# Optimization experiments

Hardware: AMD Instinct MI355X
Metric: run time of the kernel (lower is better)

## Reference

```python
import jax, jax.numpy as jnp
import numpy as np

B, L, DN, DE, DD, H = 2, 512, 512, 128, 128, 8
DK, DEH, DDH = DN // H, DE // H, DD // H
F = 2 * DK + DEH + 2 * DDH  # per-head concat feature size (176)
SLOPE = 0.2


def _kaiming(key, out_f, in_f):
    bound = np.sqrt(6.0 / ((1.0 + SLOPE ** 2) * in_f))
    return jax.random.uniform(key, (out_f, in_f), minval=-bound, maxval=bound, dtype=jnp.float32)


def lin(x, w, b):
    y = jnp.einsum('...i,oi->...o', x, w)
    return y if b is None else y + b


def setup_inputs() -> dict:
    key = jax.random.key(0)
    ks = jax.random.split(key, 16)
    inp = {
        'node_representation': jax.random.normal(ks[0], (B, L, DN), dtype=jnp.float32),
        'edge_representation': jax.random.normal(ks[1], (B, L, L, DE), dtype=jnp.float32),
        'diff_vec': jax.random.normal(ks[2], (B, L, DD), dtype=jnp.float32),
        'Wn_w': _kaiming(ks[3], DN, DN), 'Wn_b': jnp.zeros((DN,), jnp.float32),
        'We_w': _kaiming(ks[4], DE, DE), 'We_b': jnp.zeros((DE,), jnp.float32),
        'Wd_w': _kaiming(ks[5], DD, DD), 'Wd_b': jnp.zeros((DD,), jnp.float32),
        'Wh_w': _kaiming(ks[6], DK, DK), 'Wh_b': jnp.zeros((DK,), jnp.float32),
        'attn_w': _kaiming(ks[7], 1, F),
        'outn_w': _kaiming(ks[8], DN, DN), 'outn_b': jnp.zeros((DN,), jnp.float32),
        'Wn2_w': _kaiming(ks[9], DN, DN), 'Wn2_b': jnp.zeros((DN,), jnp.float32),
        'We2_w': _kaiming(ks[10], DE, DE), 'We2_b': jnp.zeros((DE,), jnp.float32),
        'Wd2_w': _kaiming(ks[11], DD, DD), 'Wd2_b': jnp.zeros((DD,), jnp.float32),
        'edge_w': _kaiming(ks[12], DEH, F), 'edge_b': jnp.zeros((DEH,), jnp.float32),
        'oute_w': _kaiming(ks[13], DE, DE), 'oute_b': jnp.zeros((DE,), jnp.float32),
    }
    return inp


def reference(node_representation, edge_representation, diff_vec,
              Wn_w, Wn_b, We_w, We_b, Wd_w, Wd_b, Wh_w, Wh_b, attn_w,
              outn_w, outn_b, Wn2_w, Wn2_b, We2_w, We2_b, Wd2_w, Wd2_b,
              edge_w, edge_b, oute_w, oute_b):
    lrelu = lambda x: jax.nn.leaky_relu(x, SLOPE)

    # ---- node update (GAT-style with concat score decomposed per term) ----
    npj = lin(node_representation, Wn_w, Wn_b).reshape(B, L, H, DK)
    epj = lin(edge_representation, We_w, We_b).reshape(B, L, L, H, DEH)
    dpj = lin(diff_vec, Wd_w, Wd_b).reshape(B, L, H, DDH)
    a = attn_w[0]  # concat order: [hi, hj, edge, di, dj]
    a_hi, a_hj = a[:DK], a[DK:2 * DK]
    a_e = a[2 * DK:2 * DK + DEH]
    a_di, a_dj = a[2 * DK + DEH:2 * DK + DEH + DDH], a[-DDH:]
    # scores[b,i,j,h]
    s = (jnp.einsum('blhd,d->blh', npj, a_hi)[:, :, None, :]
         + jnp.einsum('blhd,d->blh', npj, a_hj)[:, None, :, :]
         + jnp.einsum('blmhe,e->blmh', epj, a_e)
         + jnp.einsum('blhd,d->blh', dpj, a_di)[:, :, None, :]
         + jnp.einsum('blhd,d->blh', dpj, a_dj)[:, None, :, :])
    diag = jnp.eye(L, dtype=bool)[None, :, :, None]
    s = jnp.where(diag, -jnp.inf, s)
    probs = jax.nn.softmax(lrelu(s), axis=2)  # softmax over j
    node_wh = lin(npj, Wh_w, Wh_b)  # [B,L,H,DK]
    agg = jnp.einsum('blmh,bmhd->blhd', probs, node_wh)
    new_node = (npj + lrelu(agg)).reshape(B, L, DN)
    new_node = lin(new_node, outn_w, outn_b)

    # ---- edge update (concat-linear decomposed into per-term matmuls) ----
    np2 = lin(new_node, Wn2_w, Wn2_b).reshape(B, L, H, DK)
    ep2 = lin(edge_representation, We2_w, We2_b).reshape(B, L, L, H, DEH)
    dp2 = lin(diff_vec, Wd2_w, Wd2_b).reshape(B, L, H, DDH)
    # edge concat order: [edge, hi, hj, di, dj]
    W_e = edge_w[:, :DEH]
    W_hi = edge_w[:, DEH:DEH + DK]
    W_hj = edge_w[:, DEH + DK:DEH + 2 * DK]
    W_di = edge_w[:, DEH + 2 * DK:DEH + 2 * DK + DDH]
    W_dj = edge_w[:, -DDH:]
    e_out = (jnp.einsum('blmhe,fe->blmhf', ep2, W_e)
             + jnp.einsum('blhd,fd->blhf', np2, W_hi)[:, :, None]
             + jnp.einsum('blhd,fd->blhf', np2, W_hj)[:, None]
             + jnp.einsum('blhd,fd->blhf', dp2, W_di)[:, :, None]
             + jnp.einsum('blhd,fd->blhf', dp2, W_dj)[:, None]
             + edge_b)
    new_edge = lin(e_out.reshape(B, L, L, DE), oute_w, oute_b)
    return new_node, new_edge
```

## Files before the change

### kernel.cpp

```cpp
#include <hip/hip_runtime.h>
#include <hip/hip_bf16.h>

typedef unsigned short u16;
typedef unsigned short u16x8 __attribute__((ext_vector_type(8)));
typedef __bf16 bf16x8 __attribute__((ext_vector_type(8)));
typedef float f32x4 __attribute__((ext_vector_type(4)));

#define LRS 0.2f

__device__ __forceinline__ u16 f2b(float f) {
  __hip_bfloat16 h = __float2bfloat16(f);
  return __builtin_bit_cast(u16, h);
}

template<int K, int O, int KSEG, int R>
__device__ __forceinline__ void gemm_rowsR(const float* xr, const float* W, const float* bias,
                                           float* yl, float* yg, int ygstride) {
  constexpr int KPT = K / KSEG;
  constexpr int OPP = 256 / KSEG;
  const int t = threadIdx.x;
  const int ks = t % KSEG;
  const int oi = t / KSEG;
#pragma unroll
  for (int pass = 0; pass < O / OPP; ++pass) {
    const int o = pass * OPP + oi;
    float a[R];
#pragma unroll
    for (int r = 0; r < R; ++r) a[r] = 0.0f;
    const float* wp = W + (size_t)o * K + ks * KPT;
    const float* xb = xr + ks * KPT;
#pragma unroll 4
    for (int kc = 0; kc < KPT; kc += 4) {
      f32x4 w4 = *(const f32x4*)(wp + kc);
#pragma unroll
      for (int r = 0; r < R; ++r) {
        f32x4 x = *(const f32x4*)(xb + r * K + kc);
#pragma unroll
        for (int j = 0; j < 4; ++j) a[r] += x[j] * w4[j];
      }
    }
#pragma unroll
    for (int d = 1; d < KSEG; d <<= 1)
#pragma unroll
      for (int r = 0; r < R; ++r) a[r] += __shfl_xor(a[r], d, 64);
    if (ks == 0) {
      float bv = bias ? bias[o] : 0.0f;
#pragma unroll
      for (int r = 0; r < R; ++r) {
        float v = a[r] + bv;
        if (yl) yl[r * O + o] = v;
        if (yg) yg[(size_t)r * ygstride + o] = v;
      }
    }
  }
}

__global__ __launch_bounds__(256) void kW1(const float* We_w, const float* We_b, const float* attn,
                                           const float* We2_w, const float* We2_b,
                                           const float* edge_w, const float* edge_b,
                                           float* Mfull, u16* vb, float* cbe, float* sconst) {
  int gid = blockIdx.x * 256 + threadIdx.x;
  if (gid < 16384) {
    int hf = gid >> 7, c = gid & 127;
    int h = hf >> 4, fo = hf & 15;
    float s = 0;
    for (int e = 0; e < 16; ++e)
      s += edge_w[fo * 176 + e] * We2_w[(h * 16 + e) * 128 + c];
    Mfull[hf * 128 + c] = s;
  } else if (gid < 16384 + 2048) {
    int idx = gid - 16384;
    int c = idx >> 4, hc = idx & 15;
    float s = 0;
    if (hc < 8)
      for (int e = 0; e < 16; ++e)
        s += We_w[(hc * 16 + e) * 128 + c] * attn[128 + e];
    vb[c * 16 + hc] = f2b(s);
  } else if (gid < 18432 + 128) {
    int hf = gid - 18432;
    int h = hf >> 4, fo = hf & 15;
    float s = edge_b[fo];
    for (int e = 0; e < 16; ++e)
      s += We2_b[h * 16 + e] * edge_w[fo * 176 + e];
    cbe[hf] = s;
  } else if (gid < 18560 + 8) {
    int h = gid - 18560;
    float s = 0;
    for (int e = 0; e < 16; ++e)
      s += We_b[h * 16 + e] * attn[128 + e];
    sconst[h] = s;
  }
}

__global__ __launch_bounds__(256) void kW2(const float* oute_w, const float* Mfull, u16* Gb) {
  int gid = blockIdx.x * 256 + threadIdx.x;
  int o = gid >> 7, c = gid & 127;
  float s = 0;
  for (int k = 0; k < 128; ++k)
    s += oute_w[o * 128 + k] * Mfull[k * 128 + c];
  Gb[o * 128 + c] = f2b(s);
}

__global__ __launch_bounds__(256) void kN1(const float* node, const float* diff,
                                           const float* Wn_w, const float* Wn_b,
                                           const float* Wd_w, const float* Wd_b,
                                           const float* Wh_w, const float* Wh_b,
                                           const float* attn, const float* sconst,
                                           float* npj_g, float* nwh_g,
                                           float* srow_g, float* scol_g) {
  __shared__ float nrow[2 * 512], npjl[2 * 512], drow[2 * 128], dpjl[2 * 128];
  const int t = threadIdx.x;
  const int r0 = blockIdx.x * 2;
  *(f32x4*)&nrow[t * 4] = *(const f32x4*)(node + (size_t)r0 * 512 + t * 4);
  if (t < 64) *(f32x4*)&drow[t * 4] = *(const f32x4*)(diff + (size_t)r0 * 128 + t * 4);
  __syncthreads();
  gemm_rowsR<512, 512, 4, 2>(nrow, Wn_w, Wn_b, npjl, npj_g + (size_t)r0 * 512, 512);
  gemm_rowsR<128, 128, 4, 2>(drow, Wd_w, Wd_b, dpjl, nullptr, 0);
  __syncthreads();
  {
    int d = t & 63, hh = t >> 6;
#pragma unroll
    for (int hi = 0; hi < 2; ++hi) {
      int h = hh + hi * 4;
      float wb = Wh_b[d];
      float acc[2] = {wb, wb};
      for (int k = 0; k < 64; ++k) {
        float w = Wh_w[d * 64 + k];
#pragma unroll
        for (int r = 0; r < 2; ++r) acc[r] += npjl[r * 512 + h * 64 + k] * w;
      }
#pragma unroll
      for (int r = 0; r < 2; ++r) nwh_g[(size_t)(r0 + r) * 512 + h * 64 + d] = acc[r];
    }
  }
  if (t < 16) {
    int r = t >> 3, h = t & 7;
    float shi = 0, shj = 0, sdi = 0, sdj = 0;
    for (int d = 0; d < 64; ++d) {
      float x = npjl[r * 512 + h * 64 + d];
      shi += x * attn[d];
      shj += x * attn[64 + d];
    }
    for (int e = 0; e < 16; ++e) {
      float x = dpjl[r * 128 + h * 16 + e];
      sdi += x * attn[144 + e];
      sdj += x * attn[160 + e];
    }
    srow_g[(r0 + r) * 8 + h] = shi + sdi + sconst[h];
    scol_g[(r0 + r) * 8 + h] = shj + sdj;
  }
}

__global__ __launch_bounds__(256) void kA(const float* edge, const float* srow, const float* scol,
                                          const u16* vb, u16* P, float* invs, u16* abf) {
  __shared__ float smx[512 * 9];
  __shared__ float red[256];
  __shared__ float mxh8[8];
  const int bl = blockIdx.x;
  const int b = bl >> 9, l = bl & 511;
  const int t = threadIdx.x;
  const int lane = t & 63, w = t >> 6;
  const int colL = lane & 15, kg = lane >> 4;
  const int h = t & 7, seg = t >> 3;

  bf16x8 bfr[4];
#pragma unroll
  for (int ks = 0; ks < 4; ++ks) {
    u16x8 u;
#pragma unroll
    for (int j = 0; j < 8; ++j) u[j] = vb[(ks * 32 + kg * 8 + j) * 16 + colL];
    bfr[ks] = __builtin_bit_cast(bf16x8, u);
  }

  const float* eb = edge + (size_t)bl * 65536;
  u16* cb = abf ? abf + (size_t)bl * 65536 : nullptr;

  for (int ci = 0; ci < 8; ++ci) {
    const int r0 = w * 128 + ci * 16;
    const int row = r0 + colL;
    const float* rp = eb + (size_t)row * 128;
    f32x4 acc = {0, 0, 0, 0};
#pragma unroll
    for (int ks = 0; ks < 4; ++ks) {
      f32x4 e0 = *(const f32x4*)(rp + ks * 32 + kg * 8);
      f32x4 e1 = *(const f32x4*)(rp + ks * 32 + kg * 8 + 4);
      u16x8 a8;
#pragma unroll
      for (int j = 0; j < 4; ++j) { a8[j] = f2b(e0[j]); a8[4 + j] = f2b(e1[j]); }
      if (cb) *(u16x8*)(cb + (size_t)row * 128 + ks * 32 + kg * 8) = a8;
      acc = __builtin_amdgcn_mfma_f32_16x16x32_bf16(__builtin_bit_cast(bf16x8, a8), bfr[ks], acc, 0, 0, 0);
    }
    if (colL < 8) {
#pragma unroll
      for (int r = 0; r < 4; ++r)
        smx[(r0 + kg * 4 + r) * 9 + colL] = acc[r];
    }
  }
  __syncthreads();

  const float srh2 = srow[(size_t)bl * 8 + h];
  float mx = -__builtin_inff();
#pragma unroll 4
  for (int i = 0; i < 16; ++i) {
    int m = seg * 16 + i;
    float sv = smx[m * 9 + h] + srh2 + scol[((size_t)b * 512 + m) * 8 + h];
    sv = (m == l) ? -__builtin_inff() : (sv >= 0.0f ? sv : LRS * sv);
    smx[m * 9 + h] = sv;
    mx = fmaxf(mx, sv);
  }
  red[t] = mx;
  __syncthreads();
  if (t < 8) {
    float m2 = -__builtin_inff();
    for (int sg = 0; sg < 32; ++sg) m2 = fmaxf(m2, red[sg * 8 + t]);
    mxh8[t] = m2;
  }
  __syncthreads();
  float mh = mxh8[h];
  float smv = 0;
#pragma unroll 4
  for (int i = 0; i < 16; ++i) {
    int m = seg * 16 + i;
    float p = __expf(smx[m * 9 + h] - mh);
    smx[m * 9 + h] = p;
    smv += p;
  }
  red[t] = smv;
  __syncthreads();
  if (t < 8) {
    float s2 = 0;
    for (int sg = 0; sg < 32; ++sg) s2 += red[sg * 8 + t];
    invs[(size_t)bl * 8 + t] = 1.0f / s2;
  }
  __syncthreads();
#pragma unroll
  for (int k = 0; k < 2; ++k) {
    int c = k * 256 + t;
    int hp = c >> 6, mb = (c & 63) * 8;
    u16x8 pk;
#pragma unroll
    for (int j = 0; j < 8; ++j) pk[j] = f2b(smx[(mb + j) * 9 + hp]);
    *(u16x8*)(P + (((size_t)b * 8 + hp) * 512 + l) * 512 + mb) = pk;
  }
}

__global__ __launch_bounds__(256) void kAgg(const u16* P, const float* nwh, const float* npj,
                                            const float* invs, float* nnp) {
  __shared__ u16 Pt[8192];
  __shared__ u16 Vt[8192];
  const int bid = blockIdx.x;
  const int lt = bid & 7, h = (bid >> 3) & 7, b = bid >> 6;
  const int l0 = lt * 64;
  const int t = threadIdx.x;
  const int lane = t & 63, w = t >> 6;
  const int colL = lane & 15, kg = lane >> 4;

  f32x4 acc[4] = {};
  for (int mc = 0; mc < 4; ++mc) {
#pragma unroll
    for (int q = 0; q < 4; ++q) {
      int c = q * 256 + t;
      int row = c >> 4, cu = c & 15;
      u16x8 a8 = *(const u16x8*)(P + (((size_t)b * 8 + h) * 512 + l0 + row) * 512 + mc * 128 + cu * 8);
      *(u16x8*)(Pt + (row * 16 + (cu ^ (row & 7))) * 8) = a8;
    }
#pragma unroll
    for (int q = 0; q < 8; ++q) {
      int c = q * 256 + t;
      int m = c >> 4, d4 = (c & 15) * 4;
      f32x4 v = *(const f32x4*)(nwh + ((size_t)b * 512 + mc * 128 + m) * 512 + h * 64 + d4);
#pragma unroll
      for (int j = 0; j < 4; ++j) {
        int d = d4 + j;
        Vt[(d * 16 + ((m >> 3) ^ (d & 7))) * 8 + (m & 7)] = f2b(v[j]);
      }
    }
    __syncthreads();
#pragma unroll
    for (int kc = 0; kc < 4; ++kc) {
      int cu = kc * 4 + kg;
      int prow = w * 16 + colL;
      bf16x8 af = *(bf16x8*)(Pt + (prow * 16 + (cu ^ (prow & 7))) * 8);
#pragma unroll
      for (int n = 0; n < 4; ++n) {
        int d = n * 16 + colL;
        bf16x8 bf = *(bf16x8*)(Vt + (d * 16 + (cu ^ (d & 7))) * 8);
        acc[n] = __builtin_amdgcn_mfma_f32_16x16x32_bf16(af, bf, acc[n], 0, 0, 0);
      }
    }
    __syncthreads();
  }
#pragma unroll
  for (int r = 0; r < 4; ++r) {
    int l = l0 + w * 16 + kg * 4 + r;
    float iv = invs[((size_t)b * 512 + l) * 8 + h];
#pragma unroll
    for (int n = 0; n < 4; ++n) {
      int o = h * 64 + n * 16 + colL;
      size_t idx = ((size_t)b * 512 + l) * 512 + o;
      float a = acc[n][r] * iv;
      a = a >= 0.0f ? a : LRS * a;
      nnp[idx] = npj[idx] + a;
    }
  }
}

__global__ __launch_bounds__(256) void kN234(const float* nnp, const float* diff,
                                             const float* outn_w, const float* outn_b,
                                             const float* Wn2_w, const float* Wn2_b,
                                             const float* Wd2_w, const float* Wd2_b,
                                             const float* edge_w, const float* cbe,
                                             const float* oute_w, const float* oute_b,
                                             float* out0, float* Pl, float* Pm) {
  __shared__ float xr[2 * 512], o0l[2 * 512], np2l[2 * 512], dr[2 * 128], dp2l[2 * 128];
  __shared__ float Rls[2 * 128], Rms[2 * 128];
  const int t = threadIdx.x;
  const int r0 = blockIdx.x * 2;
  *(f32x4*)&xr[t * 4] = *(const f32x4*)(nnp + (size_t)r0 * 512 + t * 4);
  if (t < 64) *(f32x4*)&dr[t * 4] = *(const f32x4*)(diff + (size_t)r0 * 128 + t * 4);
  __syncthreads();
  gemm_rowsR<512, 512, 4, 2>(xr, outn_w, outn_b, o0l, out0 + (size_t)r0 * 512, 512);
  gemm_rowsR<128, 128, 4, 2>(dr, Wd2_w, Wd2_b, dp2l, nullptr, 0);
  __syncthreads();
  gemm_rowsR<512, 512, 4, 2>(o0l, Wn2_w, Wn2_b, np2l, nullptr, 0);
  __syncthreads();
  {
    int hf = t & 127, which = t >> 7;
    int h = hf >> 4, fo = hf & 15;
    const float* wh = edge_w + fo * 176 + 16 + which * 64;
    const float* wd = edge_w + fo * 176 + 144 + which * 16;
    float add = which ? 0.0f : cbe[hf];
    float* dst = which ? Rms : Rls;
#pragma unroll
    for (int r = 0; r < 2; ++r) {
      float a = add;
      for (int d = 0; d < 64; ++d) a += np2l[r * 512 + h * 64 + d] * wh[d];
      for (int e = 0; e < 16; ++e) a += dp2l[r * 128 + h * 16 + e] * wd[e];
      dst[r * 128 + hf] = a;
    }
  }
  __syncthreads();
  gemm_rowsR<128, 128, 4, 2>(Rls, oute_w, oute_b, nullptr, Pl + (size_t)r0 * 128, 128);
  gemm_rowsR<128, 128, 4, 2>(Rms, oute_w, nullptr, nullptr, Pm + (size_t)r0 * 128, 128);
}

__global__ __launch_bounds__(256) void kEc(const u16* Abf, const u16* Gb,
                                           const float* Pl, const float* Pm, float* oute) {
  __shared__ u16 At[8192];
  const int tile = blockIdx.x;
  const int bl = tile >> 3;
  const int b = bl >> 9;
  const int r0 = (tile & 7) * 64;
  const int t = threadIdx.x, lane = t & 63, w = t >> 6;
  const int colL = lane & 15, kg = lane >> 4;

  bf16x8 gf[2][4];
#pragma unroll
  for (int n = 0; n < 2; ++n)
#pragma unroll
    for (int ks = 0; ks < 4; ++ks) {
      int o = w * 32 + n * 16 + colL;
      gf[n][ks] = *(const bf16x8*)(Gb + o * 128 + ks * 32 + kg * 8);
    }
  f32x4 plv4[2];
#pragma unroll
  for (int n = 0; n < 2; ++n)
    plv4[n] = *(const f32x4*)(Pl + (size_t)bl * 128 + w * 32 + n * 16 + kg * 4);

  const u16* src = Abf + ((size_t)bl * 512 + r0) * 128;
#pragma unroll
  for (int q = 0; q < 4; ++q) {
    int c = q * 256 + t;
    int row = c >> 4, cu = c & 15;
    *(u16x8*)(At + (row * 16 + (cu ^ (row & 7))) * 8) = *(const u16x8*)(src + c * 8);
  }
  __syncthreads();

  f32x4 acc[4][2] = {};
#pragma unroll
  for (int i = 0; i < 4; ++i) {
#pragma unroll
    for (int ks = 0; ks < 4; ++ks) {
      int cu = ks * 4 + kg;
      int row = i * 16 + colL;
      bf16x8 af = *(bf16x8*)(At + (row * 16 + (cu ^ (row & 7))) * 8);
#pragma unroll
      for (int n = 0; n < 2; ++n)
        acc[i][n] = __builtin_amdgcn_mfma_f32_16x16x32_bf16(gf[n][ks], af, acc[i][n], 0, 0, 0);
    }
  }
  float* ob = oute + ((size_t)bl * 512 + r0) * 128;
#pragma unroll
  for (int i = 0; i < 4; ++i) {
    int m = i * 16 + colL;
    const float* pmp = Pm + ((size_t)b * 512 + r0 + m) * 128;
    float* orow = ob + (size_t)m * 128;
#pragma unroll
    for (int n = 0; n < 2; ++n) {
      int oc = w * 32 + n * 16 + kg * 4;
      f32x4 pm4 = *(const f32x4*)(pmp + oc);
      f32x4 o4;
#pragma unroll
      for (int r = 0; r < 4; ++r) o4[r] = acc[i][n][r] + plv4[n][r] + pm4[r];
      *(f32x4*)(orow + oc) = o4;
    }
  }
}

__global__ __launch_bounds__(256) void kEd(const float* edge, const u16* Gb,
                                           const float* Pl, const float* Pm, float* oute) {
  __shared__ u16 At[8192];
  const int tile = blockIdx.x;
  const int bl = tile >> 3;
  const int b = bl >> 9;
  const int r0 = (tile & 7) * 64;
  const int t = threadIdx.x, lane = t & 63, w = t >> 6;
  const int colL = lane & 15, kg = lane >> 4;
  bf16x8 gf[2][4];
#pragma unroll
  for (int n = 0; n < 2; ++n)
#pragma unroll
    for (int ks = 0; ks < 4; ++ks) {
      int o = w * 32 + n * 16 + colL;
      gf[n][ks] = *(const bf16x8*)(Gb + o * 128 + ks * 32 + kg * 8);
    }
  f32x4 plv4[2];
#pragma unroll
  for (int n = 0; n < 2; ++n)
    plv4[n] = *(const f32x4*)(Pl + (size_t)bl * 128 + w * 32 + n * 16 + kg * 4);

  const int arow = t >> 2, aseg = t & 3;
  {
    const float* p = edge + ((size_t)bl * 512 + r0 + arow) * 128 + aseg * 32;
    f32x4 v[8];
#pragma unroll
    for (int q = 0; q < 8; ++q) v[q] = *(const f32x4*)(p + q * 4);
#pragma unroll
    for (int jj = 0; jj < 4; ++jj) {
      u16x8 a8;
#pragma unroll
      for (int j2 = 0; j2 < 4; ++j2) {
        a8[j2]     = f2b(v[2 * jj][j2]);
        a8[4 + j2] = f2b(v[2 * jj + 1][j2]);
      }
      int cu = aseg * 4 + jj;
      *(u16x8*)(At + (arow * 16 + (cu ^ (arow & 7))) * 8) = a8;
    }
  }
  __syncthreads();
  f32x4 acc[4][2] = {};
#pragma unroll
  for (int i = 0; i < 4; ++i) {
#pragma unroll
    for (int ks = 0; ks < 4; ++ks) {
      int cu = ks * 4 + kg;
      int row = i * 16 + colL;
      bf16x8 af = *(bf16x8*)(At + (row * 16 + (cu ^ (row & 7))) * 8);
#pragma unroll
      for (int n = 0; n < 2; ++n)
        acc[i][n] = __builtin_amdgcn_mfma_f32_16x16x32_bf16(gf[n][ks], af, acc[i][n], 0, 0, 0);
    }
  }
  float* ob = oute + ((size_t)bl * 512 + r0) * 128;
#pragma unroll
  for (int i = 0; i < 4; ++i) {
    int m = i * 16 + colL;
    const float* pmp = Pm + ((size_t)b * 512 + r0 + m) * 128;
    float* orow = ob + (size_t)m * 128;
#pragma unroll
    for (int n = 0; n < 2; ++n) {
      int oc = w * 32 + n * 16 + kg * 4;
      f32x4 pm4 = *(const f32x4*)(pmp + oc);
      f32x4 o4;
#pragma unroll
      for (int r = 0; r < 4; ++r) o4[r] = acc[i][n][r] + plv4[n][r] + pm4[r];
      *(f32x4*)(orow + oc) = o4;
    }
  }
}

extern "C" void kernel_launch(void* const* d_in, const int* in_sizes, int n_in,
                              void* d_out, int out_size, void* d_ws, size_t ws_size,
                              hipStream_t stream) {
  (void)in_sizes; (void)n_in; (void)out_size;
  const float* node   = (const float*)d_in[0];
  const float* edge   = (const float*)d_in[1];
  const float* diff   = (const float*)d_in[2];
  const float* Wn_w   = (const float*)d_in[3];
  const float* Wn_b   = (const float*)d_in[4];
  const float* We_w   = (const float*)d_in[5];
  const float* We_b   = (const float*)d_in[6];
  const float* Wd_w   = (const float*)d_in[7];
  const float* Wd_b   = (const float*)d_in[8];
  const float* Wh_w   = (const float*)d_in[9];
  const float* Wh_b   = (const float*)d_in[10];
  const float* attn   = (const float*)d_in[11];
  const float* outn_w = (const float*)d_in[12];
  const float* outn_b = (const float*)d_in[13];
  const float* Wn2_w  = (const float*)d_in[14];
  const float* Wn2_b  = (const float*)d_in[15];
  const float* We2_w  = (const float*)d_in[16];
  const float* We2_b  = (const float*)d_in[17];
  const float* Wd2_w  = (const float*)d_in[18];
  const float* Wd2_b  = (const float*)d_in[19];
  const float* edge_w = (const float*)d_in[20];
  const float* edge_b = (const float*)d_in[21];
  const float* oute_w = (const float*)d_in[22];
  const float* oute_b = (const float*)d_in[23];

  float* out0 = (float*)d_out;
  float* out1 = out0 + 524288;

  float* f = (float*)d_ws;
  size_t off = 0;
  auto alloc = [&](size_t n) { float* p = f + off; off += (n + 7) & ~(size_t)7; return p; };
  float* npj    = alloc(524288);
  float* nwh    = alloc(524288);
  float* srow   = alloc(8192);
  float* scol   = alloc(8192);
  float* sconst = alloc(8);
  float* cbe    = alloc(128);
  float* Mfull  = alloc(16384);
  float* nnp    = alloc(524288);
  float* Pl     = alloc(131072);
  float* Pm     = alloc(131072);
  float* invs   = alloc(8192);
  u16* vb = (u16*)(f + off); off += 1024;
  u16* Gb = (u16*)(f + off); off += 8192;
  u16* P  = (u16*)(f + off); off += 2097152;
  const size_t abf_elems = (size_t)2 * 512 * 512 * 128;
  bool cache = ws_size >= off * 4 + abf_elems * 2 + 256;
  u16* Abf = cache ? (u16*)(f + off) : nullptr;

  hipLaunchKernelGGL(kW1, dim3(73), dim3(256), 0, stream,
                     We_w, We_b, attn, We2_w, We2_b, edge_w, edge_b, Mfull, vb, cbe, sconst);
  hipLaunchKernelGGL(kW2, dim3(64), dim3(256), 0, stream, oute_w, Mfull, Gb);
  hipLaunchKernelGGL(kN1, dim3(512), dim3(256), 0, stream,
                     node, diff, Wn_w, Wn_b, Wd_w, Wd_b, Wh_w, Wh_b, attn, sconst,
                     npj, nwh, srow, scol);
  hipLaunchKernelGGL(kA, dim3(1024), dim3(256), 0, stream,
                     edge, srow, scol, vb, P, invs, Abf);
  hipLaunchKernelGGL(kAgg, dim3(128), dim3(256), 0, stream, P, nwh, npj, invs, nnp);
  hipLaunchKernelGGL(kN234, dim3(512), dim3(256), 0, stream,
                     nnp, diff, outn_w, outn_b, Wn2_w, Wn2_b, Wd2_w, Wd2_b,
                     edge_w, cbe, oute_w, oute_b, out0, Pl, Pm);
  if (cache)
    hipLaunchKernelGGL(kEc, dim3(8192), dim3(256), 0, stream, Abf, Gb, Pl, Pm, out1);
  else
    hipLaunchKernelGGL(kEd, dim3(8192), dim3(256), 0, stream, edge, Gb, Pl, Pm, out1);
}
```

Baseline: 523.0 us.

## Split edge-score kernel into FP32 row-dot pass and separate softmax kernel

```diff
diff --git a/kernel.cpp b/kernel.cpp
--- a/kernel.cpp
+++ b/kernel.cpp
@@ -58,7 +58,7 @@
 __global__ __launch_bounds__(256) void kW1(const float* We_w, const float* We_b, const float* attn,
                                            const float* We2_w, const float* We2_b,
                                            const float* edge_w, const float* edge_b,
-                                           float* Mfull, u16* vb, float* cbe, float* sconst) {
+                                           float* Mfull, float* vf, float* cbe, float* sconst) {
   int gid = blockIdx.x * 256 + threadIdx.x;
   if (gid < 16384) {
     int hf = gid >> 7, c = gid & 127;
@@ -67,23 +67,22 @@
     for (int e = 0; e < 16; ++e)
       s += edge_w[fo * 176 + e] * We2_w[(h * 16 + e) * 128 + c];
     Mfull[hf * 128 + c] = s;
-  } else if (gid < 16384 + 2048) {
+  } else if (gid < 16384 + 1024) {
     int idx = gid - 16384;
-    int c = idx >> 4, hc = idx & 15;
+    int c = idx >> 3, h = idx & 7;
     float s = 0;
-    if (hc < 8)
-      for (int e = 0; e < 16; ++e)
-        s += We_w[(hc * 16 + e) * 128 + c] * attn[128 + e];
-    vb[c * 16 + hc] = f2b(s);
-  } else if (gid < 18432 + 128) {
-    int hf = gid - 18432;
+    for (int e = 0; e < 16; ++e)
+      s += We_w[(h * 16 + e) * 128 + c] * attn[128 + e];
+    vf[c * 8 + h] = s;
+  } else if (gid < 17408 + 128) {
+    int hf = gid - 17408;
     int h = hf >> 4, fo = hf & 15;
     float s = edge_b[fo];
     for (int e = 0; e < 16; ++e)
       s += We2_b[h * 16 + e] * edge_w[fo * 176 + e];
     cbe[hf] = s;
-  } else if (gid < 18560 + 8) {
-    int h = gid - 18560;
+  } else if (gid < 17536 + 8) {
+    int h = gid - 17536;
     float s = 0;
     for (int e = 0; e < 16; ++e)
       s += We_b[h * 16 + e] * attn[128 + e];
@@ -150,53 +149,79 @@
   }
 }
 
-__global__ __launch_bounds__(256) void kA(const float* edge, const float* srow, const float* scol,
-                                          const u16* vb, u16* P, float* invs, u16* abf) {
+__global__ __launch_bounds__(256) void kS(const float* __restrict__ edge,
+                                          const float* __restrict__ vf,
+                                          float* __restrict__ se, u16* __restrict__ abf) {
+  __shared__ float vl[1024];
+  const int t = threadIdx.x;
+  *(f32x4*)&vl[t * 4] = *(const f32x4*)(vf + t * 4);
+  __syncthreads();
+  const size_t row = (size_t)blockIdx.x * 256 + t;
+  const float* rp = edge + row * 128;
+  u16* cp = abf ? abf + row * 128 : nullptr;
+  f32x4 A[8], B[8];
+#pragma unroll
+  for (int q = 0; q < 8; ++q) A[q] = *(const f32x4*)(rp + q * 4);
+#pragma unroll
+  for (int q = 0; q < 8; ++q) B[q] = *(const f32x4*)(rp + 32 + q * 4);
+  f32x4 acc0 = {0, 0, 0, 0}, acc1 = {0, 0, 0, 0};
+
+#define PROCG(BUF, CB)                                                     \
+  {                                                                        \
+    _Pragma("unroll") for (int q = 0; q < 8; ++q) {                        \
+      f32x4 v = BUF[q];                                                    \
+      int c = CB + q * 4;                                                  \
+      _Pragma("unroll") for (int j = 0; j < 4; ++j) {                      \
+        f32x4 w0 = *(const f32x4*)&vl[(c + j) * 8];                        \
+        f32x4 w1 = *(const f32x4*)&vl[(c + j) * 8 + 4];                    \
+        acc0 += v[j] * w0;                                                 \
+        acc1 += v[j] * w1;                                                 \
+      }                                                                    \
+    }                                                                      \
+    if (cp) {                                                              \
+      _Pragma("unroll") for (int q = 0; q < 8; q += 2) {                   \
+        u16x8 pk;                                                          \
+        _Pragma("unroll") for (int j = 0; j < 4; ++j) {                    \
+          pk[j] = f2b(BUF[q][j]);                                          \
+          pk[4 + j] = f2b(BUF[q + 1][j]);                                  \
+        }                                                                  \
+        *(u16x8*)(cp + CB + q * 4) = pk;                                   \
+      }                                                                    \
+    }                                                                      \
+  }
+
+  PROCG(A, 0);
+#pragma unroll
+  for (int q = 0; q < 8; ++q) A[q] = *(const f32x4*)(rp + 64 + q * 4);
+  PROCG(B, 32);
+#pragma unroll
+  for (int q = 0; q < 8; ++q) B[q] = *(const f32x4*)(rp + 96 + q * 4);
+  PROCG(A, 64);
+  PROCG(B, 96);
+#undef PROCG
+  *(f32x4*)(se + row * 8)     = acc0;
+  *(f32x4*)(se + row * 8 + 4) = acc1;
+}
+
+__global__ __launch_bounds__(256) void kSM(const float* se, const float* srow, const float* scol,
+                                           u16* P, float* invs) {
   __shared__ float smx[512 * 9];
   __shared__ float red[256];
   __shared__ float mxh8[8];
   const int bl = blockIdx.x;
   const int b = bl >> 9, l = bl & 511;
   const int t = threadIdx.x;
-  const int lane = t & 63, w = t >> 6;
-  const int colL = lane & 15, kg = lane >> 4;
   const int h = t & 7, seg = t >> 3;
-
-  bf16x8 bfr[4];
-#pragma unroll
-  for (int ks = 0; ks < 4; ++ks) {
-    u16x8 u;
-#pragma unroll
-    for (int j = 0; j < 8; ++j) u[j] = vb[(ks * 32 + kg * 8 + j) * 16 + colL];
-    bfr[ks] = __builtin_bit_cast(bf16x8, u);
-  }
-
-  const float* eb = edge + (size_t)bl * 65536;
-  u16* cb = abf ? abf + (size_t)bl * 65536 : nullptr;
-
-  for (int ci = 0; ci < 8; ++ci) {
-    const int r0 = w * 128 + ci * 16;
-    const int row = r0 + colL;
-    const float* rp = eb + (size_t)row * 128;
-    f32x4 acc = {0, 0, 0, 0};
-#pragma unroll
-    for (int ks = 0; ks < 4; ++ks) {
-      f32x4 e0 = *(const f32x4*)(rp + ks * 32 + kg * 8);
-      f32x4 e1 = *(const f32x4*)(rp + ks * 32 + kg * 8 + 4);
-      u16x8 a8;
-#pragma unroll
-      for (int j = 0; j < 4; ++j) { a8[j] = f2b(e0[j]); a8[4 + j] = f2b(e1[j]); }
-      if (cb) *(u16x8*)(cb + (size_t)row * 128 + ks * 32 + kg * 8) = a8;
-      acc = __builtin_amdgcn_mfma_f32_16x16x32_bf16(__builtin_bit_cast(bf16x8, a8), bfr[ks], acc, 0, 0, 0);
-    }
-    if (colL < 8) {
-#pragma unroll
-      for (int r = 0; r < 4; ++r)
-        smx[(r0 + kg * 4 + r) * 9 + colL] = acc[r];
-    }
-  }
-  __syncthreads();
-
+  const float* sb = se + (size_t)bl * 4096;
+#pragma unroll
+  for (int k = 0; k < 4; ++k) {
+    int idx = k * 1024 + t * 4;
+    int m = idx >> 3, hh = idx & 7;
+    f32x4 v = *(const f32x4*)(sb + idx);
+#pragma unroll
+    for (int j = 0; j < 4; ++j) smx[m * 9 + hh + j] = v[j];
+  }
+  __syncthreads();
   const float srh2 = srow[(size_t)bl * 8 + h];
   float mx = -__builtin_inff();
 #pragma unroll 4
@@ -524,21 +549,22 @@
   float* Pl     = alloc(131072);
   float* Pm     = alloc(131072);
   float* invs   = alloc(8192);
-  u16* vb = (u16*)(f + off); off += 1024;
+  float* vf     = alloc(1024);
+  float* se     = alloc(4194304);
   u16* Gb = (u16*)(f + off); off += 8192;
   u16* P  = (u16*)(f + off); off += 2097152;
   const size_t abf_elems = (size_t)2 * 512 * 512 * 128;
   bool cache = ws_size >= off * 4 + abf_elems * 2 + 256;
   u16* Abf = cache ? (u16*)(f + off) : nullptr;
 
-  hipLaunchKernelGGL(kW1, dim3(73), dim3(256), 0, stream,
-                     We_w, We_b, attn, We2_w, We2_b, edge_w, edge_b, Mfull, vb, cbe, sconst);
+  hipLaunchKernelGGL(kW1, dim3(70), dim3(256), 0, stream,
+                     We_w, We_b, attn, We2_w, We2_b, edge_w, edge_b, Mfull, vf, cbe, sconst);
   hipLaunchKernelGGL(kW2, dim3(64), dim3(256), 0, stream, oute_w, Mfull, Gb);
   hipLaunchKernelGGL(kN1, dim3(512), dim3(256), 0, stream,
                      node, diff, Wn_w, Wn_b, Wd_w, Wd_b, Wh_w, Wh_b, attn, sconst,
                      npj, nwh, srow, scol);
-  hipLaunchKernelGGL(kA, dim3(1024), dim3(256), 0, stream,
-                     edge, srow, scol, vb, P, invs, Abf);
+  hipLaunchKernelGGL(kS, dim3(2048), dim3(256), 0, stream, edge, vf, se, Abf);
+  hipLaunchKernelGGL(kSM, dim3(1024), dim3(256), 0, stream, se, srow, scol, P, invs);
   hipLaunchKernelGGL(kAgg, dim3(128), dim3(256), 0, stream, P, nwh, npj, invs, nnp);
   hipLaunchKernelGGL(kN234, dim3(512), dim3(256), 0, stream,
                      nnp, diff, outn_w, outn_b, Wn2_w, Wn2_b, Wd2_w, Wd2_b,
```

Measured after the change: 1.155 ms. 121% more time.

## Drop bf16 edge cache and double-buffer edge loads in attention kernel

Applied to the files above, without the earlier changes.

```diff
diff --git a/kernel.cpp b/kernel.cpp
--- a/kernel.cpp
+++ b/kernel.cpp
@@ -2,6 +2,7 @@
 #include <hip/hip_bf16.h>
 
 typedef unsigned short u16;
+typedef unsigned short u16x4 __attribute__((ext_vector_type(4)));
 typedef unsigned short u16x8 __attribute__((ext_vector_type(8)));
 typedef __bf16 bf16x8 __attribute__((ext_vector_type(8)));
 typedef float f32x4 __attribute__((ext_vector_type(4)));
@@ -151,7 +152,7 @@
 }
 
 __global__ __launch_bounds__(256) void kA(const float* edge, const float* srow, const float* scol,
-                                          const u16* vb, u16* P, float* invs, u16* abf) {
+                                          const u16* vb, u16* P, float* invs) {
   __shared__ float smx[512 * 9];
   __shared__ float red[256];
   __shared__ float mxh8[8];
@@ -161,6 +162,7 @@
   const int lane = t & 63, w = t >> 6;
   const int colL = lane & 15, kg = lane >> 4;
   const int h = t & 7, seg = t >> 3;
+  const int rbase = w * 128;
 
   bf16x8 bfr[4];
 #pragma unroll
@@ -172,29 +174,45 @@
   }
 
   const float* eb = edge + (size_t)bl * 65536;
-  u16* cb = abf ? abf + (size_t)bl * 65536 : nullptr;
-
-  for (int ci = 0; ci < 8; ++ci) {
-    const int r0 = w * 128 + ci * 16;
-    const int row = r0 + colL;
-    const float* rp = eb + (size_t)row * 128;
-    f32x4 acc = {0, 0, 0, 0};
-#pragma unroll
-    for (int ks = 0; ks < 4; ++ks) {
-      f32x4 e0 = *(const f32x4*)(rp + ks * 32 + kg * 8);
-      f32x4 e1 = *(const f32x4*)(rp + ks * 32 + kg * 8 + 4);
-      u16x8 a8;
-#pragma unroll
-      for (int j = 0; j < 4; ++j) { a8[j] = f2b(e0[j]); a8[4 + j] = f2b(e1[j]); }
-      if (cb) *(u16x8*)(cb + (size_t)row * 128 + ks * 32 + kg * 8) = a8;
-      acc = __builtin_amdgcn_mfma_f32_16x16x32_bf16(__builtin_bit_cast(bf16x8, a8), bfr[ks], acc, 0, 0, 0);
-    }
-    if (colL < 8) {
-#pragma unroll
-      for (int r = 0; r < 4; ++r)
-        smx[(r0 + kg * 4 + r) * 9 + colL] = acc[r];
-    }
-  }
+
+#define LOADC(BUF, CI)                                                       \
+  {                                                                          \
+    const float* rp = eb + (size_t)(rbase + (CI) * 16 + colL) * 128 + kg * 8;\
+    _Pragma("unroll") for (int ks = 0; ks < 4; ++ks) {                       \
+      BUF[2 * ks]     = *(const f32x4*)(rp + ks * 32);                       \
+      BUF[2 * ks + 1] = *(const f32x4*)(rp + ks * 32 + 4);                   \
+    }                                                                        \
+  }
+#define PROCC(BUF, CI)                                                       \
+  {                                                                          \
+    f32x4 acc = {0, 0, 0, 0};                                                \
+    _Pragma("unroll") for (int ks = 0; ks < 4; ++ks) {                       \
+      u16x8 a8;                                                              \
+      _Pragma("unroll") for (int j = 0; j < 4; ++j) {                        \
+        a8[j]     = f2b(BUF[2 * ks][j]);                                     \
+        a8[4 + j] = f2b(BUF[2 * ks + 1][j]);                                 \
+      }                                                                      \
+      acc = __builtin_amdgcn_mfma_f32_16x16x32_bf16(                         \
+          __builtin_bit_cast(bf16x8, a8), bfr[ks], acc, 0, 0, 0);            \
+    }                                                                        \
+    if (colL < 8) {                                                          \
+      _Pragma("unroll") for (int r = 0; r < 4; ++r)                          \
+        smx[(rbase + (CI) * 16 + kg * 4 + r) * 9 + colL] = acc[r];           \
+    }                                                                        \
+  }
+
+  f32x4 A[8], B[8];
+  LOADC(A, 0); LOADC(B, 1);
+  PROCC(A, 0); LOADC(A, 2);
+  PROCC(B, 1); LOADC(B, 3);
+  PROCC(A, 2); LOADC(A, 4);
+  PROCC(B, 3); LOADC(B, 5);
+  PROCC(A, 4); LOADC(A, 6);
+  PROCC(B, 5); LOADC(B, 7);
+  PROCC(A, 6);
+  PROCC(B, 7);
+#undef LOADC
+#undef PROCC
   __syncthreads();
 
   const float srh2 = srow[(size_t)bl * 8 + h];
@@ -343,8 +361,8 @@
   gemm_rowsR<128, 128, 4, 2>(Rms, oute_w, nullptr, nullptr, Pm + (size_t)r0 * 128, 128);
 }
 
-__global__ __launch_bounds__(256) void kEc(const u16* Abf, const u16* Gb,
-                                           const float* Pl, const float* Pm, float* oute) {
+__global__ __launch_bounds__(256) void kE(const float* edge, const u16* Gb,
+                                          const float* Pl, const float* Pm, float* oute) {
   __shared__ u16 At[8192];
   const int tile = blockIdx.x;
   const int bl = tile >> 3;
@@ -366,12 +384,17 @@
   for (int n = 0; n < 2; ++n)
     plv4[n] = *(const f32x4*)(Pl + (size_t)bl * 128 + w * 32 + n * 16 + kg * 4);
 
-  const u16* src = Abf + ((size_t)bl * 512 + r0) * 128;
-#pragma unroll
-  for (int q = 0; q < 4; ++q) {
-    int c = q * 256 + t;
-    int row = c >> 4, cu = c & 15;
-    *(u16x8*)(At + (row * 16 + (cu ^ (row & 7))) * 8) = *(const u16x8*)(src + c * 8);
+  const float* src = edge + ((size_t)bl * 512 + r0) * 128;
+#pragma unroll
+  for (int k = 0; k < 8; ++k) {
+    int fidx = t * 4 + k * 1024;
+    f32x4 v = *(const f32x4*)(src + fidx);
+    int row = fidx >> 7, col = fidx & 127;
+    int cu = col >> 3, sub = col & 7;
+    u16x4 pk;
+#pragma unroll
+    for (int j = 0; j < 4; ++j) pk[j] = f2b(v[j]);
+    *(u16x4*)(At + (row * 16 + (cu ^ (row & 7))) * 8 + sub) = pk;
   }
   __syncthreads();
 
@@ -406,82 +429,10 @@
   }
 }
 
-__global__ __launch_bounds__(256) void kEd(const float* edge, const u16* Gb,
-                                           const float* Pl, const float* Pm, float* oute) {
-  __shared__ u16 At[8192];
-  const int tile = blockIdx.x;
-  const int bl = tile >> 3;
-  const int b = bl >> 9;
-  const int r0 = (tile & 7) * 64;
-  const int t = threadIdx.x, lane = t & 63, w = t >> 6;
-  const int colL = lane & 15, kg = lane >> 4;
-  bf16x8 gf[2][4];
-#pragma unroll
-  for (int n = 0; n < 2; ++n)
-#pragma unroll
-    for (int ks = 0; ks < 4; ++ks) {
-      int o = w * 32 + n * 16 + colL;
-      gf[n][ks] = *(const bf16x8*)(Gb + o * 128 + ks * 32 + kg * 8);
-    }
-  f32x4 plv4[2];
-#pragma unroll
-  for (int n = 0; n < 2; ++n)
-    plv4[n] = *(const f32x4*)(Pl + (size_t)bl * 128 + w * 32 + n * 16 + kg * 4);
-
-  const int arow = t >> 2, aseg = t & 3;
-  {
-    const float* p = edge + ((size_t)bl * 512 + r0 + arow) * 128 + aseg * 32;
-    f32x4 v[8];
-#pragma unroll
-    for (int q = 0; q < 8; ++q) v[q] = *(const f32x4*)(p + q * 4);
-#pragma unroll
-    for (int jj = 0; jj < 4; ++jj) {
-      u16x8 a8;
-#pragma unroll
-      for (int j2 = 0; j2 < 4; ++j2) {
-        a8[j2]     = f2b(v[2 * jj][j2]);
-        a8[4 + j2] = f2b(v[2 * jj + 1][j2]);
-      }
-      int cu = aseg * 4 + jj;
-      *(u16x8*)(At + (arow * 16 + (cu ^ (arow & 7))) * 8) = a8;
-    }
-  }
-  __syncthreads();
-  f32x4 acc[4][2] = {};
-#pragma unroll
-  for (int i = 0; i < 4; ++i) {
-#pragma unroll
-    for (int ks = 0; ks < 4; ++ks) {
-      int cu = ks * 4 + kg;
-      int row = i * 16 + colL;
-      bf16x8 af = *(bf16x8*)(At + (row * 16 + (cu ^ (row & 7))) * 8);
-#pragma unroll
-      for (int n = 0; n < 2; ++n)
-        acc[i][n] = __builtin_amdgcn_mfma_f32_16x16x32_bf16(gf[n][ks], af, acc[i][n], 0, 0, 0);
-    }
-  }
-  float* ob = oute + ((size_t)bl * 512 + r0) * 128;
-#pragma unroll
-  for (int i = 0; i < 4; ++i) {
-    int m = i * 16 + colL;
-    const float* pmp = Pm + ((size_t)b * 512 + r0 + m) * 128;
-    float* orow = ob + (size_t)m * 128;
-#pragma unroll
-    for (int n = 0; n < 2; ++n) {
-      int oc = w * 32 + n * 16 + kg * 4;
-      f32x4 pm4 = *(const f32x4*)(pmp + oc);
-      f32x4 o4;
-#pragma unroll
-      for (int r = 0; r < 4; ++r) o4[r] = acc[i][n][r] + plv4[n][r] + pm4[r];
-      *(f32x4*)(orow + oc) = o4;
-    }
-  }
-}
-
 extern "C" void kernel_launch(void* const* d_in, const int* in_sizes, int n_in,
                               void* d_out, int out_size, void* d_ws, size_t ws_size,
                               hipStream_t stream) {
-  (void)in_sizes; (void)n_in; (void)out_size;
+  (void)in_sizes; (void)n_in; (void)out_size; (void)ws_size;
   const float* node   = (const float*)d_in[0];
   const float* edge   = (const float*)d_in[1];
   const float* diff   = (const float*)d_in[2];
@@ -527,9 +478,6 @@
   u16* vb = (u16*)(f + off); off += 1024;
   u16* Gb = (u16*)(f + off); off += 8192;
   u16* P  = (u16*)(f + off); off += 2097152;
-  const size_t abf_elems = (size_t)2 * 512 * 512 * 128;
-  bool cache = ws_size >= off * 4 + abf_elems * 2 + 256;
-  u16* Abf = cache ? (u16*)(f + off) : nullptr;
 
   hipLaunchKernelGGL(kW1, dim3(73), dim3(256), 0, stream,
                      We_w, We_b, attn, We2_w, We2_b, edge_w, edge_b, Mfull, vb, cbe, sconst);
@@ -538,13 +486,10 @@
                      node, diff, Wn_w, Wn_b, Wd_w, Wd_b, Wh_w, Wh_b, attn, sconst,
                      npj, nwh, srow, scol);
   hipLaunchKernelGGL(kA, dim3(1024), dim3(256), 0, stream,
-                     edge, srow, scol, vb, P, invs, Abf);
+                     edge, srow, scol, vb, P, invs);
   hipLaunchKernelGGL(kAgg, dim3(128), dim3(256), 0, stream, P, nwh, npj, invs, nnp);
   hipLaunchKernelGGL(kN234, dim3(512), dim3(256), 0, stream,
                      nnp, diff, outn_w, outn_b, Wn2_w, Wn2_b, Wd2_w, Wd2_b,
                      edge_w, cbe, oute_w, oute_b, out0, Pl, Pm);
-  if (cache)
-    hipLaunchKernelGGL(kEc, dim3(8192), dim3(256), 0, stream, Abf, Gb, Pl, Pm, out1);
-  else
-    hipLaunchKernelGGL(kEd, dim3(8192), dim3(256), 0, stream, edge, Gb, Pl, Pm, out1);
-}
+  hipLaunchKernelGGL(kE, dim3(8192), dim3(256), 0, stream, edge, Gb, Pl, Pm, out1);
+}
```

New measurement: 465.9 us. 1.12x faster.
